# Performance work log

Measured on AMD Instinct MI355X. Metric: run time of the kernel, lower is better.

The kernel has to match this reference:

```python
import jax, jax.numpy as jnp
import numpy as np

B_IMG = 2
N_PROP = 2000
N_GT = 16
C_FEAT = 256
H_FEAT = 128
W_FEAT = 128
IMG = 1024.0
NUM_CLASSES = 2
BG_THRESH = 0.5          # fg==bg==0.5 -> BETWEEN_THRESHOLDS band is empty
BPI = 512                # batch_size_per_image
NUM_POS_MAX = int(BPI * 0.25)
ENC_W = (1.0, 1.0, 1.0, 1.0, 1.0)
SCALE = 1.0 / 8.0        # feature stride
POOL = 7
SR = 2                   # sampling_ratio
BETA = 1.0 / 9.0
HID = 1024


def _make_boxes(key, shape_prefix, img=IMG):
    kc, ks = jax.random.split(key)
    c = jax.random.uniform(kc, shape_prefix + (2,), minval=0.0, maxval=img)
    s = jax.random.uniform(ks, shape_prefix + (2,), minval=20.0, maxval=200.0)
    lo = jnp.clip(c - 0.5 * s, 0.0, img - 2.0)
    hi = jnp.clip(c + 0.5 * s, lo + 1.0, img)
    return jnp.concatenate([lo, hi], axis=-1)  # [.., x1,y1,x2,y2]


def setup_inputs():
    key = jax.random.key(0)
    ks = jax.random.split(key, 12)
    features = jax.random.normal(ks[0], (B_IMG, C_FEAT, H_FEAT, W_FEAT), dtype=jnp.float32)
    proposals = _make_boxes(ks[1], (B_IMG, N_PROP))
    gt_boxes = _make_boxes(ks[2], (B_IMG, N_GT))
    gt_labels = jax.random.randint(ks[3], (B_IMG, N_GT), 1, NUM_CLASSES, dtype=jnp.int32)
    ka, kb, kt = jax.random.split(ks[4], 3)
    a = jax.random.uniform(ka, (B_IMG, N_GT), minval=10.0, maxval=60.0)
    b = jax.random.uniform(kb, (B_IMG, N_GT), minval=5.0, maxval=30.0)
    th = jax.random.uniform(kt, (B_IMG, N_GT), minval=-np.pi / 2, maxval=np.pi / 2)
    exy = 0.5 * (gt_boxes[..., :2] + gt_boxes[..., 2:])
    gt_ellipses = jnp.stack([a, b, exy[..., 0], exy[..., 1], th], axis=-1)
    d_in = C_FEAT * POOL * POOL
    w1 = jax.random.normal(ks[5], (d_in, HID), dtype=jnp.float32) * 0.02
    b1 = jnp.zeros((HID,), jnp.float32)
    w2 = jax.random.normal(ks[6], (HID, HID), dtype=jnp.float32) * 0.02
    b2 = jnp.zeros((HID,), jnp.float32)
    wc = jax.random.normal(ks[7], (HID, NUM_CLASSES), dtype=jnp.float32) * 0.02
    bc = jnp.zeros((NUM_CLASSES,), jnp.float32)
    wr = jax.random.normal(ks[8], (HID, NUM_CLASSES * 6), dtype=jnp.float32) * 0.02
    br = jnp.zeros((NUM_CLASSES * 6,), jnp.float32)
    return dict(features=features, proposals=proposals, gt_boxes=gt_boxes,
                gt_labels=gt_labels, gt_ellipses=gt_ellipses,
                w1=w1, b1=b1, w2=w2, b2=b2, wc=wc, bc=bc, wr=wr, br=br)


def box_iou(b1, b2):  # [G,4], [P,4] -> [G,P]
    a1 = (b1[:, 2] - b1[:, 0]) * (b1[:, 3] - b1[:, 1])
    a2 = (b2[:, 2] - b2[:, 0]) * (b2[:, 3] - b2[:, 1])
    lt = jnp.maximum(b1[:, None, :2], b2[None, :, :2])
    rb = jnp.minimum(b1[:, None, 2:], b2[None, :, 2:])
    wh = jnp.clip(rb - lt, 0.0)
    inter = wh[..., 0] * wh[..., 1]
    return inter / (a1[:, None] + a2[None, :] - inter)


def encode_ellipses(ell, boxes):  # ell [..,5]=(a,b,cx,cy,theta), boxes [..,4] -> [..,6]
    a, b, ex, ey, th = (ell[..., i] for i in range(5))
    w = jnp.maximum(boxes[..., 2] - boxes[..., 0], 1.0)
    h = jnp.maximum(boxes[..., 3] - boxes[..., 1], 1.0)
    cx = 0.5 * (boxes[..., 0] + boxes[..., 2])
    cy = 0.5 * (boxes[..., 1] + boxes[..., 3])
    wx, wy, wa, wb, wt = ENC_W
    dx = wx * (ex - cx) / w
    dy = wy * (ey - cy) / h
    da = wa * jnp.log(jnp.maximum(2.0 * a, 1e-3) / w)
    db = wb * jnp.log(jnp.maximum(2.0 * b, 1e-3) / h)
    return jnp.stack([dx, dy, da, db, wt * jnp.sin(2.0 * th), wt * jnp.cos(2.0 * th)], axis=-1)


def roi_align(fmap, rois):  # [C,H,W], [R,4] -> [R,C,POOL,POOL]
    C, H, W = fmap.shape
    r = rois * SCALE
    x1, y1, x2, y2 = r[:, 0], r[:, 1], r[:, 2], r[:, 3]
    bw = jnp.maximum(x2 - x1, 1.0) / POOL
    bh = jnp.maximum(y2 - y1, 1.0) / POOL
    S = POOL * SR
    off = (jnp.arange(S, dtype=jnp.float32) + 0.5) / SR  # bin-unit sample offsets
    ys = jnp.clip(y1[:, None] + off[None, :] * bh[:, None], 0.0, H - 1.0)  # [R,S]
    xs = jnp.clip(x1[:, None] + off[None, :] * bw[:, None], 0.0, W - 1.0)
    y0 = jnp.clip(jnp.floor(ys), 0, H - 2).astype(jnp.int32)
    x0 = jnp.clip(jnp.floor(xs), 0, W - 2).astype(jnp.int32)
    ly = ys - y0
    lx = xs - x0
    Ya, Yb = y0[:, :, None], (y0 + 1)[:, :, None]  # [R,S,1]
    Xa, Xb = x0[:, None, :], (x0 + 1)[:, None, :]  # [R,1,S]
    v00 = fmap[:, Ya, Xa]; v01 = fmap[:, Ya, Xb]   # [C,R,S,S]
    v10 = fmap[:, Yb, Xa]; v11 = fmap[:, Yb, Xb]
    wy1 = ly[:, :, None]; wy0 = 1.0 - wy1
    wx1 = lx[:, None, :]; wx0 = 1.0 - wx1
    val = v00 * (wy0 * wx0) + v01 * (wy0 * wx1) + v10 * (wy1 * wx0) + v11 * (wy1 * wx1)
    R = rois.shape[0]
    pooled = val.reshape(C, R, POOL, SR, POOL, SR).mean(axis=(3, 5))
    return pooled.transpose(1, 0, 2, 3)


def reference(features, proposals, gt_boxes, gt_labels, gt_ellipses,
              w1, b1, w2, b2, wc, bc, wr, br):
    B = features.shape[0]
    # add_gt_proposals
    props = jnp.concatenate([proposals, gt_boxes], axis=1)            # [B,P,4]
    # assign_targets_to_proposals: IoU + Matcher (fg=bg=0.5)
    iou = jax.vmap(box_iou)(gt_boxes, props)                          # [B,G,P]
    matched_vals = iou.max(axis=1)
    matches = iou.argmax(axis=1)                                      # [B,P]
    lab = jnp.take_along_axis(gt_labels, matches, axis=1)
    lab = jnp.where(matched_vals < BG_THRESH, 0, lab)                 # background
    # BalancedPositiveNegativeSampler (deterministic, fixed-shape):
    # cap positives at NUM_POS_MAX by random rank, fill rest with random negatives
    rand = jax.random.uniform(jax.random.key(42), lab.shape)
    is_pos = lab > 0
    is_neg = lab == 0
    pos_s = jnp.where(is_pos, rand, -1e9)
    rank = jnp.argsort(jnp.argsort(-pos_s, axis=1), axis=1)
    capped = is_pos & (rank < NUM_POS_MAX)
    prio = jnp.where(capped, rand + 2.0, jnp.where(is_neg, rand, -1e9))
    _, idx = jax.lax.top_k(prio, BPI)                                 # [B,512]
    boxes = jnp.take_along_axis(props, idx[..., None], axis=1)        # [B,512,4]
    labels = jnp.take_along_axis(lab, idx, axis=1)                    # [B,512]
    m = jnp.take_along_axis(matches, idx, axis=1)
    ell = jnp.take_along_axis(gt_ellipses, m[..., None], axis=1)      # [B,512,5]
    targets = encode_ellipses(ell, boxes)                             # [B,512,6]
    # RoIAlign + TwoMLPHead + predictor
    pooled = jax.vmap(roi_align)(features, boxes)                     # [B,512,C,7,7]
    N = B * BPI
    x = pooled.reshape(N, -1)
    x = jax.nn.relu(x @ w1 + b1)
    x = jax.nn.relu(x @ w2 + b2)
    logits = x @ wc + bc                                              # [N,2]
    reg = (x @ wr + br).reshape(N, NUM_CLASSES, 6)
    # ellipse_rcnn_loss
    labels_f = labels.reshape(N)
    t = targets.reshape(N, 6)
    ce = -jnp.take_along_axis(jax.nn.log_softmax(logits, axis=-1), labels_f[:, None], axis=1).mean()
    pred = jnp.take_along_axis(reg, labels_f[:, None, None], axis=1)[:, 0]  # [N,6]
    d = jnp.abs(pred - t)
    sl1 = jnp.where(d < BETA, 0.5 * d * d / BETA, d - 0.5 * BETA)
    reg_loss = jnp.sum(sl1 * (labels_f > 0)[:, None].astype(sl1.dtype)) / N
    return jnp.stack([ce, reg_loss])
```

## Files before the change

### kernel.cpp

```cpp
#include <hip/hip_runtime.h>
#include <hip/hip_bf16.h>
#include <math.h>

#define B_IMG   2
#define N_PROP  2000
#define N_GT    16
#define NPROPS  2016
#define C_FEAT  256
#define H_FEAT  128
#define W_FEAT  128
#define HWF     (H_FEAT*W_FEAT)
#define POOL    7
#define BPI     512
#define NPOSMAX 128
#define NSEL    (B_IMG*BPI)
#define K1      (C_FEAT*POOL*POOL)
#define K1P     12800
#define HID     1024
#define NHEAD   14
#define SPLITK1 16
#define SPLITK2 4

typedef short bf16x8f __attribute__((ext_vector_type(8)));
typedef float f32x4f  __attribute__((ext_vector_type(4)));
typedef short short4v __attribute__((ext_vector_type(4)));

__device__ __forceinline__ void threefry2x32(unsigned k0, unsigned k1,
                                             unsigned& x0, unsigned& x1) {
  unsigned ks[3] = {k0, k1, k0 ^ k1 ^ 0x1BD11BDAu};
  const int R0[4] = {13, 15, 26, 6};
  const int R1[4] = {17, 29, 16, 24};
  x0 += ks[0]; x1 += ks[1];
#pragma unroll
  for (int g = 0; g < 5; g++) {
    const int* rot = (g & 1) ? R1 : R0;
#pragma unroll
    for (int r = 0; r < 4; r++) {
      x0 += x1;
      x1 = (x1 << rot[r]) | (x1 >> (32 - rot[r]));
      x1 ^= x0;
    }
    x0 += ks[(g + 1) % 3];
    x1 += ks[(g + 2) % 3] + (unsigned)(g + 1);
  }
}

__global__ __launch_bounds__(256) void k_sample(const float* __restrict__ proposals,
                                                const float* __restrict__ gt_boxes,
                                                const int* __restrict__ gt_labels,
                                                float* __restrict__ prio,
                                                int* __restrict__ plab,
                                                int* __restrict__ matches) {
  __shared__ float rs[NPROPS];
  __shared__ short pos_i[NPROPS];
  __shared__ float pos_r[NPROPS];
  __shared__ float gtb[N_GT * 4];
  __shared__ int   gtl[N_GT];
  __shared__ int   cnt;
  int b = blockIdx.x;
  int tid = threadIdx.x;
  int base = b * NPROPS;
  if (tid == 0) cnt = 0;
  if (tid < N_GT * 4) gtb[tid] = gt_boxes[b * N_GT * 4 + tid];
  if (tid < N_GT) gtl[tid] = gt_labels[b * N_GT + tid];
  __syncthreads();
  for (int i = tid; i < NPROPS; i += 256) {
    unsigned x0 = 0u, x1 = (unsigned)(base + i);
    threefry2x32(0u, 42u, x0, x1);
    unsigned bits = x0 ^ x1;
    float r = __uint_as_float((bits >> 9) | 0x3F800000u) - 1.0f;
    rs[i] = r;
    float p0, p1, p2, p3;
    if (i < N_PROP) {
      const float4 v = *(const float4*)(proposals + ((size_t)b * N_PROP + i) * 4);
      p0 = v.x; p1 = v.y; p2 = v.z; p3 = v.w;
    } else {
      const float* g = &gtb[(i - N_PROP) * 4];
      p0 = g[0]; p1 = g[1]; p2 = g[2]; p3 = g[3];
    }
    float a2 = (p2 - p0) * (p3 - p1);
    float best = -1.0f; int bg = 0;
#pragma unroll
    for (int g = 0; g < N_GT; g++) {
      float g0 = gtb[g * 4], g1 = gtb[g * 4 + 1], g2 = gtb[g * 4 + 2], g3 = gtb[g * 4 + 3];
      float a1 = (g2 - g0) * (g3 - g1);
      float wx = fmaxf(fminf(g2, p2) - fmaxf(g0, p0), 0.0f);
      float wy = fmaxf(fminf(g3, p3) - fmaxf(g1, p1), 0.0f);
      float inter = wx * wy;
      float iou = inter / (a1 + a2 - inter);
      if (iou > best) { best = iou; bg = g; }
    }
    matches[base + i] = bg;
    int lab = (best < 0.5f) ? 0 : gtl[bg];
    plab[base + i] = lab;
    if (lab > 0) {
      int s = atomicAdd(&cnt, 1);
      pos_i[s] = (short)i; pos_r[s] = r;
    }
  }
  __syncthreads();
  int P = cnt;
  for (int s = tid; s < P; s += 256) {
    int i = pos_i[s]; float ri = pos_r[s];
    int ch = 0;
    for (int j = 0; j < P; j++) {
      float rj = pos_r[j]; int ij = pos_i[j];
      ch += (rj > ri || (rj == ri && ij < i)) ? 1 : 0;
    }
    rs[i] = (ch < NPOSMAX) ? (ri + 2.0f) : -1000000000.0f;
  }
  __syncthreads();
  for (int i = tid; i < NPROPS; i += 256) prio[base + i] = rs[i];
}

__global__ __launch_bounds__(256) void k_select(const float* __restrict__ prio,
    const float* __restrict__ proposals, const float* __restrict__ gt_boxes,
    const int* __restrict__ matches, const int* __restrict__ plab,
    const float* __restrict__ gt_ell,
    float* __restrict__ sel_boxes, int* __restrict__ sel_labels,
    float* __restrict__ targets) {
  int tid = threadIdx.x;
  int wave = tid >> 6, lane = tid & 63;
  int b = blockIdx.y;
  int base = b * NPROPS;
  int i = blockIdx.x * 4 + wave;
  float pi = prio[base + i];
  int rank = 0;
  for (int j = lane; j < NPROPS; j += 64) {
    float pj = prio[base + j];
    rank += (pj > pi || (pj == pi && j < i)) ? 1 : 0;
  }
#pragma unroll
  for (int off = 32; off > 0; off >>= 1) rank += __shfl_down(rank, off);
  if (lane != 0 || rank >= BPI) return;
  int slot = b * BPI + rank;
  float p0, p1, p2, p3;
  if (i < N_PROP) {
    const float* p = proposals + ((size_t)b * N_PROP + i) * 4;
    p0 = p[0]; p1 = p[1]; p2 = p[2]; p3 = p[3];
  } else {
    const float* p = gt_boxes + ((size_t)b * N_GT + (i - N_PROP)) * 4;
    p0 = p[0]; p1 = p[1]; p2 = p[2]; p3 = p[3];
  }
  sel_boxes[slot * 4 + 0] = p0;
  sel_boxes[slot * 4 + 1] = p1;
  sel_boxes[slot * 4 + 2] = p2;
  sel_boxes[slot * 4 + 3] = p3;
  int lb = plab[base + i];
  sel_labels[slot] = lb;
  int m = matches[base + i];
  const float* e = gt_ell + ((size_t)b * N_GT + m) * 5;
  float ea = e[0], eb = e[1], ex = e[2], ey = e[3], eth = e[4];
  float w = fmaxf(p2 - p0, 1.0f), h = fmaxf(p3 - p1, 1.0f);
  float cx = 0.5f * (p0 + p2), cy = 0.5f * (p1 + p3);
  float* t = targets + (size_t)slot * 6;
  t[0] = (ex - cx) / w;
  t[1] = (ey - cy) / h;
  t[2] = logf(fmaxf(2.0f * ea, 0.001f) / w);
  t[3] = logf(fmaxf(2.0f * eb, 0.001f) / h);
  t[4] = sinf(2.0f * eth);
  t[5] = cosf(2.0f * eth);
}

__global__ __launch_bounds__(256) void k_transpose(const float* __restrict__ in,
                                                   __hip_bfloat16* __restrict__ out) {
  __shared__ float tile[64][65];
  int b = blockIdx.z;
  int s0 = blockIdx.x * 64;
  int c0 = blockIdx.y * 64;
  const float* src = in + (size_t)b * C_FEAT * HWF;
  __hip_bfloat16* dst = out + (size_t)b * HWF * C_FEAT;
  int t = threadIdx.x;
  int hw4 = (t & 15) * 4;
  int cr  = t >> 4;
#pragma unroll
  for (int p = 0; p < 4; p++) {
    int c = cr + p * 16;
    float4 v = *(const float4*)(src + (size_t)(c0 + c) * HWF + s0 + hw4);
    tile[hw4 + 0][c] = v.x;
    tile[hw4 + 1][c] = v.y;
    tile[hw4 + 2][c] = v.z;
    tile[hw4 + 3][c] = v.w;
  }
  __syncthreads();
  int c4 = (t & 15) * 4;
  int hr = t >> 4;
#pragma unroll
  for (int p = 0; p < 4; p++) {
    int hw = hr + p * 16;
    __hip_bfloat16 o[4] = {__float2bfloat16(tile[hw][c4]), __float2bfloat16(tile[hw][c4 + 1]),
                           __float2bfloat16(tile[hw][c4 + 2]), __float2bfloat16(tile[hw][c4 + 3])};
    *(short4v*)(dst + (size_t)(s0 + hw) * C_FEAT + c0 + c4) = *(short4v*)o;
  }
}

template <int PERM>
__global__ __launch_bounds__(256) void k_castT(const float* __restrict__ W,
                                               __hip_bfloat16* __restrict__ WT,
                                               int Kout) {
  __shared__ float t[64][65];
  int p  = blockIdx.z;
  int c0 = blockIdx.x * 64;
  int n0 = blockIdx.y * 64;
  int tx = threadIdx.x & 63, ty = threadIdx.x >> 6;
#pragma unroll
  for (int i = ty; i < 64; i += 4) {
    int krow = PERM ? ((c0 + i) * 49 + p) : (c0 + i);
    t[i][tx] = W[(size_t)krow * HID + n0 + tx];
  }
  __syncthreads();
#pragma unroll
  for (int i = ty; i < 64; i += 4) {
    int kx = PERM ? (p * 256 + c0 + tx) : (c0 + tx);
    WT[(size_t)(n0 + i) * Kout + kx] = __float2bfloat16(t[tx][i]);
  }
}

__global__ __launch_bounds__(256) void k_pad(__hip_bfloat16* __restrict__ Xb,
                                             __hip_bfloat16* __restrict__ W1T) {
  __hip_bfloat16* buf = blockIdx.y ? W1T : Xb;
  int t = blockIdx.x * 256 + threadIdx.x;
  int row = t >> 6;
  int col4 = (t & 63) << 2;
  short4v z = {0, 0, 0, 0};
  *(short4v*)(buf + (size_t)row * K1P + K1 + col4) = z;
}

__global__ __launch_bounds__(256) void k_roialign(const __hip_bfloat16* __restrict__ featT,
                                                  const float* __restrict__ sel_boxes,
                                                  __hip_bfloat16* __restrict__ X) {
  int n = blockIdx.x;
  int py = blockIdx.y;
  int t = threadIdx.x;
  int lane = t & 63, sub = t >> 6;
  int c = lane << 2;
  int b = n >> 9;
  const float* bx = sel_boxes + (size_t)n * 4;
  float x1 = bx[0] * 0.125f, y1 = bx[1] * 0.125f;
  float x2 = bx[2] * 0.125f, y2 = bx[3] * 0.125f;
  float bw = fmaxf(x2 - x1, 1.0f) / 7.0f;
  float bh = fmaxf(y2 - y1, 1.0f) / 7.0f;
  const __hip_bfloat16* base = featT + (size_t)b * HWF * C_FEAT;
  int y0A[2]; float lyA[2];
#pragma unroll
  for (int sy = 0; sy < 2; sy++) {
    float off = ((float)(py * 2 + sy) + 0.5f) * 0.5f;
    float ys = fminf(fmaxf(y1 + off * bh, 0.0f), 127.0f);
    int y0 = (int)fminf(fmaxf(floorf(ys), 0.0f), 126.0f);
    y0A[sy] = y0; lyA[sy] = ys - (float)y0;
  }
#pragma unroll
  for (int pass = 0; pass < 2; pass++) {
    int px = sub + (pass << 2);
    if (px >= 7) break;
    float acc[4] = {0.0f, 0.0f, 0.0f, 0.0f};
#pragma unroll
    for (int sx = 0; sx < 2; sx++) {
      float off = ((float)(px * 2 + sx) + 0.5f) * 0.5f;
      float xs = fminf(fmaxf(x1 + off * bw, 0.0f), 127.0f);
      int x0 = (int)fminf(fmaxf(floorf(xs), 0.0f), 126.0f);
      float lx = xs - (float)x0;
#pragma unroll
      for (int sy = 0; sy < 2; sy++) {
        int y0 = y0A[sy]; float ly = lyA[sy];
        const __hip_bfloat16* p = base + ((size_t)(y0 * W_FEAT + x0)) * C_FEAT + c;
        short4v s00 = *(const short4v*)p;
        short4v s01 = *(const short4v*)(p + C_FEAT);
        short4v s10 = *(const short4v*)(p + W_FEAT * C_FEAT);
        short4v s11 = *(const short4v*)(p + W_FEAT * C_FEAT + C_FEAT);
        float w00 = (1.0f - ly) * (1.0f - lx), w01 = (1.0f - ly) * lx;
        float w10 = ly * (1.0f - lx), w11 = ly * lx;
#pragma unroll
        for (int q = 0; q < 4; q++) {
          float v00 = __uint_as_float(((unsigned)(unsigned short)s00[q]) << 16);
          float v01 = __uint_as_float(((unsigned)(unsigned short)s01[q]) << 16);
          float v10 = __uint_as_float(((unsigned)(unsigned short)s10[q]) << 16);
          float v11 = __uint_as_float(((unsigned)(unsigned short)s11[q]) << 16);
          acc[q] += v00 * w00 + v01 * w01 + v10 * w10 + v11 * w11;
        }
      }
    }
    __hip_bfloat16 o[4] = {__float2bfloat16(acc[0] * 0.25f), __float2bfloat16(acc[1] * 0.25f),
                           __float2bfloat16(acc[2] * 0.25f), __float2bfloat16(acc[3] * 0.25f)};
    *(short4v*)&X[(size_t)n * K1P + (size_t)(py * 7 + px) * C_FEAT + c] = *(short4v*)o;
  }
}

__device__ __forceinline__ void gld_lds16(const __hip_bfloat16* g, __hip_bfloat16* l) {
  __builtin_amdgcn_global_load_lds(
      (const __attribute__((address_space(1))) void*)g,
      (__attribute__((address_space(3))) void*)l, 16, 0, 0);
}

template <int MODE>
__global__ __launch_bounds__(MODE == 1 ? 512 : 256)
void k_mfma_gemm(const __hip_bfloat16* __restrict__ A,
                 const __hip_bfloat16* __restrict__ BT,
                 float* __restrict__ P, int K, int KC) {
  const int AM  = (MODE == 1) ? 256 : 128;
  const int TPB = AM * 2;
  __shared__ __align__(16) __hip_bfloat16 As[AM * 32];
  __shared__ __align__(16) __hip_bfloat16 Bs[128 * 32];
  int lin = blockIdx.x;
  int n0, m0, kz;
  if (MODE == 1) {
    int c = lin & 7, h = lin >> 8, q = (lin >> 3) & 31;
    kz = c + (h << 3);
    n0 = (q & 7) * 128;
    m0 = (q >> 3) * 256;
  } else {
    int c = lin & 7;
    kz = c >> 1;
    int q = (lin >> 3) + ((c & 1) << 5);
    n0 = (q & 7) * 128;
    m0 = (q >> 3) * 128;
  }
  int tid = threadIdx.x;
  int kbeg = kz * KC;
  int srow = tid >> 2;
  int scs  = tid & 3;
  int sg   = scs ^ (srow & 3);
  int scol = sg << 3;
  int wave = tid >> 6, lane = tid & 63;
  const int WMW = AM / 64;
  int wm = (wave % WMW) * 64, wn = (wave / WMW) * 64;
  int lm = lane & 15, quad = lane >> 4;
  int fco = ((quad ^ (lm & 3)) << 3);
  f32x4f acc[4][4] = {};
  for (int k0 = kbeg; k0 < kbeg + KC; k0 += 32) {
    __syncthreads();
#pragma unroll
    for (int r0 = 0; r0 < AM; r0 += TPB / 4)
      gld_lds16(A + (size_t)(m0 + r0 + srow) * K + k0 + scol, &As[(r0 + srow) * 32 + scs * 8]);
#pragma unroll
    for (int r0 = 0; r0 < 128; r0 += TPB / 4)
      gld_lds16(BT + (size_t)(n0 + r0 + srow) * K + k0 + scol, &Bs[(r0 + srow) * 32 + scs * 8]);
    __syncthreads();
    bf16x8f af[4], bf[4];
#pragma unroll
    for (int i = 0; i < 4; i++)
      af[i] = *(const bf16x8f*)&As[(wm + i * 16 + lm) * 32 + fco];
#pragma unroll
    for (int j = 0; j < 4; j++)
      bf[j] = *(const bf16x8f*)&Bs[(wn + j * 16 + lm) * 32 + fco];
#pragma unroll
    for (int i = 0; i < 4; i++)
#pragma unroll
      for (int j = 0; j < 4; j++)
        acc[i][j] = __builtin_amdgcn_mfma_f32_16x16x32_bf16(af[i], bf[j], acc[i][j], 0, 0, 0);
  }
#pragma unroll
  for (int i = 0; i < 4; i++)
#pragma unroll
    for (int j = 0; j < 4; j++) {
      float* base = P + ((size_t)kz << 20)
                      + (size_t)(m0 + wm + i * 16 + quad * 4) * HID
                      + (n0 + wn + j * 16 + lm);
#pragma unroll
      for (int r = 0; r < 4; r++) base[(size_t)r * HID] = acc[i][j][r];
    }
}

template <int Z>
__global__ __launch_bounds__(256) void k_reduce(const float* __restrict__ P,
                                                const float* __restrict__ bias,
                                                __hip_bfloat16* __restrict__ O) {
  int idx4 = blockIdx.x * 256 + threadIdx.x;
  int m = idx4 >> 8;
  int n4 = (idx4 & 255) << 2;
  float4 s = *(const float4*)(bias + n4);
#pragma unroll
  for (int z = 0; z < Z; z++) {
    float4 p = *(const float4*)(P + ((size_t)z << 20) + ((size_t)m << 10) + n4);
    s.x += p.x; s.y += p.y; s.z += p.z; s.w += p.w;
  }
  __hip_bfloat16 t[4] = {__float2bfloat16(fmaxf(s.x, 0.0f)), __float2bfloat16(fmaxf(s.y, 0.0f)),
                         __float2bfloat16(fmaxf(s.z, 0.0f)), __float2bfloat16(fmaxf(s.w, 0.0f))};
  *(short4v*)(O + ((size_t)m << 10) + n4) = *(short4v*)t;
}

__global__ __launch_bounds__(256) void k_reduce_head(const float* __restrict__ P,
                                                     const float* __restrict__ bias,
                                                     const float* __restrict__ wc,
                                                     const float* __restrict__ bc,
                                                     const float* __restrict__ wr,
                                                     const float* __restrict__ br,
                                                     float* __restrict__ Y) {
  __shared__ float part[4][NHEAD];
  int m = blockIdx.x, tid = threadIdx.x;
  int n4 = tid << 2;
  float4 s = *(const float4*)(bias + n4);
#pragma unroll
  for (int z = 0; z < SPLITK2; z++) {
    float4 p = *(const float4*)(P + ((size_t)z << 20) + ((size_t)m << 10) + n4);
    s.x += p.x; s.y += p.y; s.z += p.z; s.w += p.w;
  }
  float hv4[4] = {fmaxf(s.x, 0.0f), fmaxf(s.y, 0.0f), fmaxf(s.z, 0.0f), fmaxf(s.w, 0.0f)};
  float a[NHEAD];
#pragma unroll
  for (int j = 0; j < NHEAD; j++) a[j] = 0.0f;
#pragma unroll
  for (int q = 0; q < 4; q++) {
    int kk = n4 + q;
    float hv = hv4[q];
    float2 wcv = *(const float2*)(wc + kk * 2);
    float4 w0 = *(const float4*)(wr + kk * 12);
    float4 w1 = *(const float4*)(wr + kk * 12 + 4);
    float4 w2 = *(const float4*)(wr + kk * 12 + 8);
    a[0] += hv * wcv.x;  a[1] += hv * wcv.y;
    a[2] += hv * w0.x;   a[3] += hv * w0.y;  a[4] += hv * w0.z;  a[5] += hv * w0.w;
    a[6] += hv * w1.x;   a[7] += hv * w1.y;  a[8] += hv * w1.z;  a[9] += hv * w1.w;
    a[10] += hv * w2.x;  a[11] += hv * w2.y; a[12] += hv * w2.z; a[13] += hv * w2.w;
  }
#pragma unroll
  for (int j = 0; j < NHEAD; j++)
#pragma unroll
    for (int off = 32; off > 0; off >>= 1) a[j] += __shfl_down(a[j], off);
  int wave = tid >> 6, lane = tid & 63;
  if (lane == 0)
#pragma unroll
    for (int j = 0; j < NHEAD; j++) part[wave][j] = a[j];
  __syncthreads();
  if (tid < NHEAD) {
    float v = part[0][tid] + part[1][tid] + part[2][tid] + part[3][tid];
    Y[(size_t)m * NHEAD + tid] = v + ((tid < 2) ? bc[tid] : br[tid - 2]);
  }
}

__global__ __launch_bounds__(1024) void k_loss(const float* __restrict__ Y,
                                               const int* __restrict__ sel_labels,
                                               const float* __restrict__ T,
                                               float* __restrict__ out) {
  __shared__ float sc[1024];
  __shared__ float sr[1024];
  int n = threadIdx.x;
  float l0 = Y[(size_t)n * NHEAD + 0], l1 = Y[(size_t)n * NHEAD + 1];
  int lb = sel_labels[n];
  float mx = fmaxf(l0, l1);
  float lse = mx + logf(expf(l0 - mx) + expf(l1 - mx));
  float ce = lse - (lb ? l1 : l0);
  float reg = 0.0f;
  if (lb > 0) {
    const float beta = 1.0f / 9.0f;
    const float* pr = Y + (size_t)n * NHEAD + 2 + lb * 6;
    const float* t = T + (size_t)n * 6;
#pragma unroll
    for (int j = 0; j < 6; j++) {
      float d = fabsf(pr[j] - t[j]);
      reg += (d < beta) ? (0.5f * d * d / beta) : (d - 0.5f * beta);
    }
  }
  sc[n] = ce; sr[n] = reg;
  __syncthreads();
  for (int s = 512; s > 0; s >>= 1) {
    if (n < s) { sc[n] += sc[n + s]; sr[n] += sr[n + s]; }
    __syncthreads();
  }
  if (n == 0) {
    out[0] = sc[0] * (1.0f / 1024.0f);
    out[1] = sr[0] * (1.0f / 1024.0f);
  }
}

extern "C" void kernel_launch(void* const* d_in, const int* in_sizes, int n_in,
                              void* d_out, int out_size, void* d_ws, size_t ws_size,
                              hipStream_t stream) {
  const float* features  = (const float*)d_in[0];
  const float* proposals = (const float*)d_in[1];
  const float* gt_boxes  = (const float*)d_in[2];
  const int*   gt_labels = (const int*)d_in[3];
  const float* gt_ell    = (const float*)d_in[4];
  const float* w1 = (const float*)d_in[5];
  const float* b1 = (const float*)d_in[6];
  const float* w2 = (const float*)d_in[7];
  const float* b2 = (const float*)d_in[8];
  const float* wc = (const float*)d_in[9];
  const float* bc = (const float*)d_in[10];
  const float* wr = (const float*)d_in[11];
  const float* br = (const float*)d_in[12];
  float* out = (float*)d_out;

  char* ws = (char*)d_ws;
  size_t off = 0;
  auto take = [&](size_t bytes) -> void* {
    void* p = ws + off;
    off = (off + bytes + 255) & ~(size_t)255;
    return p;
  };
  float* P = (float*)take((size_t)SPLITK1 * HID * HID * 4);
  __hip_bfloat16* featT = (__hip_bfloat16*)P;
  __hip_bfloat16* Xb  = (__hip_bfloat16*)take((size_t)NSEL * K1P * 2);
  float* Y   = (float*)Xb;
  __hip_bfloat16* W1T = (__hip_bfloat16*)take((size_t)HID * K1P * 2);
  __hip_bfloat16* W2T = (__hip_bfloat16*)take((size_t)HID * HID * 2);
  __hip_bfloat16* H1b = (__hip_bfloat16*)take((size_t)NSEL * HID * 2);
  int*   matches   = (int*)take((size_t)B_IMG * NPROPS * 4);
  int*   plab      = (int*)take((size_t)B_IMG * NPROPS * 4);
  float* prio      = (float*)take((size_t)B_IMG * NPROPS * 4);
  float* sel_boxes = (float*)take((size_t)NSEL * 4 * 4);
  int*   sel_lab   = (int*)take((size_t)NSEL * 4);
  float* targets   = (float*)take((size_t)NSEL * 6 * 4);

  k_sample<<<B_IMG, 256, 0, stream>>>(proposals, gt_boxes, gt_labels, prio, plab, matches);
  k_pad<<<dim3(256, 2), 256, 0, stream>>>(Xb, W1T);
  k_transpose<<<dim3(HWF / 64, C_FEAT / 64, B_IMG), 256, 0, stream>>>(features, featT);
  k_castT<1><<<dim3(C_FEAT / 64, HID / 64, 49), 256, 0, stream>>>(w1, W1T, K1P);
  k_castT<0><<<dim3(HID / 64, HID / 64, 1), 256, 0, stream>>>(w2, W2T, HID);
  k_select<<<dim3(NPROPS / 4, B_IMG), 256, 0, stream>>>(prio, proposals, gt_boxes,
                                                        matches, plab, gt_ell,
                                                        sel_boxes, sel_lab, targets);
  k_roialign<<<dim3(NSEL, POOL), 256, 0, stream>>>(featT, sel_boxes, Xb);

  k_mfma_gemm<1><<<512, 512, 0, stream>>>(Xb, W1T, P, K1P, K1P / SPLITK1);
  k_reduce<SPLITK1><<<1024, 256, 0, stream>>>(P, b1, H1b);
  k_mfma_gemm<2><<<256, 256, 0, stream>>>(H1b, W2T, P, HID, HID / SPLITK2);
  k_reduce_head<<<1024, 256, 0, stream>>>(P, b2, wc, bc, wr, br, Y);

  k_loss<<<1, 1024, 0, stream>>>(Y, sel_lab, targets, out);
}
```

Measured before the change: 287.3 us.

## Fuse preprocessing kernels and store split-K partials as tiled bf16

Merges the sampling, feature transpose, weight cast and padding kernels into one launch that dispatches on block index, cutting launch overhead and serial gaps. GEMM split-K partials are now written as bf16 in a fragment-native tiled layout instead of fp32 row-major, which halves partial-sum traffic and makes the stores contiguous. The reducers are rewritten to index that layout. The second GEMM uses split-K 8 instead of 4 for more blocks. Rounding partials to bf16 before reduction loses accuracy.

Result: faster. 239.2 us (-16.7%).

```diff
diff --git a/kernel.cpp b/kernel.cpp
--- a/kernel.cpp
+++ b/kernel.cpp
@@ -19,7 +19,7 @@
 #define HID     1024
 #define NHEAD   14
 #define SPLITK1 16
-#define SPLITK2 4
+#define SPLITK2 8
 
 typedef short bf16x8f __attribute__((ext_vector_type(8)));
 typedef float f32x4f  __attribute__((ext_vector_type(4)));
@@ -45,72 +45,151 @@
   }
 }
 
-__global__ __launch_bounds__(256) void k_sample(const float* __restrict__ proposals,
-                                                const float* __restrict__ gt_boxes,
-                                                const int* __restrict__ gt_labels,
-                                                float* __restrict__ prio,
-                                                int* __restrict__ plab,
-                                                int* __restrict__ matches) {
-  __shared__ float rs[NPROPS];
-  __shared__ short pos_i[NPROPS];
-  __shared__ float pos_r[NPROPS];
-  __shared__ float gtb[N_GT * 4];
-  __shared__ int   gtl[N_GT];
-  __shared__ int   cnt;
-  int b = blockIdx.x;
+#define PRE_SAMPLE   2
+#define PRE_TRANS    (PRE_SAMPLE + 2048)
+#define PRE_CAST1    (PRE_TRANS + 3136)
+#define PRE_CAST0    (PRE_CAST1 + 256)
+#define PRE_TOTAL    (PRE_CAST0 + 512)
+
+__global__ __launch_bounds__(256) void k_pre(const float* __restrict__ proposals,
+                                             const float* __restrict__ gt_boxes,
+                                             const int* __restrict__ gt_labels,
+                                             const float* __restrict__ features,
+                                             const float* __restrict__ w1,
+                                             const float* __restrict__ w2,
+                                             float* __restrict__ prio,
+                                             int* __restrict__ plab,
+                                             int* __restrict__ matches,
+                                             __hip_bfloat16* __restrict__ featT,
+                                             __hip_bfloat16* __restrict__ W1T,
+                                             __hip_bfloat16* __restrict__ W2T,
+                                             __hip_bfloat16* __restrict__ Xb) {
+  __shared__ __align__(16) char smem[20800];
+  int bid = blockIdx.x;
   int tid = threadIdx.x;
-  int base = b * NPROPS;
-  if (tid == 0) cnt = 0;
-  if (tid < N_GT * 4) gtb[tid] = gt_boxes[b * N_GT * 4 + tid];
-  if (tid < N_GT) gtl[tid] = gt_labels[b * N_GT + tid];
-  __syncthreads();
-  for (int i = tid; i < NPROPS; i += 256) {
-    unsigned x0 = 0u, x1 = (unsigned)(base + i);
-    threefry2x32(0u, 42u, x0, x1);
-    unsigned bits = x0 ^ x1;
-    float r = __uint_as_float((bits >> 9) | 0x3F800000u) - 1.0f;
-    rs[i] = r;
-    float p0, p1, p2, p3;
-    if (i < N_PROP) {
-      const float4 v = *(const float4*)(proposals + ((size_t)b * N_PROP + i) * 4);
-      p0 = v.x; p1 = v.y; p2 = v.z; p3 = v.w;
-    } else {
-      const float* g = &gtb[(i - N_PROP) * 4];
-      p0 = g[0]; p1 = g[1]; p2 = g[2]; p3 = g[3];
-    }
-    float a2 = (p2 - p0) * (p3 - p1);
-    float best = -1.0f; int bg = 0;
-#pragma unroll
-    for (int g = 0; g < N_GT; g++) {
-      float g0 = gtb[g * 4], g1 = gtb[g * 4 + 1], g2 = gtb[g * 4 + 2], g3 = gtb[g * 4 + 3];
-      float a1 = (g2 - g0) * (g3 - g1);
-      float wx = fmaxf(fminf(g2, p2) - fmaxf(g0, p0), 0.0f);
-      float wy = fmaxf(fminf(g3, p3) - fmaxf(g1, p1), 0.0f);
-      float inter = wx * wy;
-      float iou = inter / (a1 + a2 - inter);
-      if (iou > best) { best = iou; bg = g; }
-    }
-    matches[base + i] = bg;
-    int lab = (best < 0.5f) ? 0 : gtl[bg];
-    plab[base + i] = lab;
-    if (lab > 0) {
-      int s = atomicAdd(&cnt, 1);
-      pos_i[s] = (short)i; pos_r[s] = r;
-    }
-  }
-  __syncthreads();
-  int P = cnt;
-  for (int s = tid; s < P; s += 256) {
-    int i = pos_i[s]; float ri = pos_r[s];
-    int ch = 0;
-    for (int j = 0; j < P; j++) {
-      float rj = pos_r[j]; int ij = pos_i[j];
-      ch += (rj > ri || (rj == ri && ij < i)) ? 1 : 0;
-    }
-    rs[i] = (ch < NPOSMAX) ? (ri + 2.0f) : -1000000000.0f;
-  }
-  __syncthreads();
-  for (int i = tid; i < NPROPS; i += 256) prio[base + i] = rs[i];
+  if (bid < PRE_SAMPLE) {
+    float* rs    = (float*)smem;
+    float* pos_r = (float*)(smem + 8064);
+    short* pos_i = (short*)(smem + 16128);
+    float* gtb   = (float*)(smem + 20160);
+    int*   gtl   = (int*)(smem + 20416);
+    int*   cnt   = (int*)(smem + 20480);
+    int b = bid;
+    int base = b * NPROPS;
+    if (tid == 0) *cnt = 0;
+    if (tid < N_GT * 4) gtb[tid] = gt_boxes[b * N_GT * 4 + tid];
+    if (tid < N_GT) gtl[tid] = gt_labels[b * N_GT + tid];
+    __syncthreads();
+    for (int i = tid; i < NPROPS; i += 256) {
+      unsigned x0 = 0u, x1 = (unsigned)(base + i);
+      threefry2x32(0u, 42u, x0, x1);
+      unsigned bits = x0 ^ x1;
+      float r = __uint_as_float((bits >> 9) | 0x3F800000u) - 1.0f;
+      rs[i] = r;
+      float p0, p1, p2, p3;
+      if (i < N_PROP) {
+        const float4 v = *(const float4*)(proposals + ((size_t)b * N_PROP + i) * 4);
+        p0 = v.x; p1 = v.y; p2 = v.z; p3 = v.w;
+      } else {
+        const float* g = &gtb[(i - N_PROP) * 4];
+        p0 = g[0]; p1 = g[1]; p2 = g[2]; p3 = g[3];
+      }
+      float a2 = (p2 - p0) * (p3 - p1);
+      float best = -1.0f; int bg = 0;
+#pragma unroll
+      for (int g = 0; g < N_GT; g++) {
+        float g0 = gtb[g*4], g1 = gtb[g*4+1], g2 = gtb[g*4+2], g3 = gtb[g*4+3];
+        float a1 = (g2 - g0) * (g3 - g1);
+        float wx = fmaxf(fminf(g2, p2) - fmaxf(g0, p0), 0.0f);
+        float wy = fmaxf(fminf(g3, p3) - fmaxf(g1, p1), 0.0f);
+        float inter = wx * wy;
+        float iou = inter / (a1 + a2 - inter);
+        if (iou > best) { best = iou; bg = g; }
+      }
+      matches[base + i] = bg;
+      int lab = (best < 0.5f) ? 0 : gtl[bg];
+      plab[base + i] = lab;
+      if (lab > 0) {
+        int s = atomicAdd(cnt, 1);
+        pos_i[s] = (short)i; pos_r[s] = r;
+      }
+    }
+    __syncthreads();
+    int P = *cnt;
+    for (int s = tid; s < P; s += 256) {
+      int i = pos_i[s]; float ri = pos_r[s];
+      int ch = 0;
+      for (int j = 0; j < P; j++) {
+        float rj = pos_r[j]; int ij = pos_i[j];
+        ch += (rj > ri || (rj == ri && ij < i)) ? 1 : 0;
+      }
+      rs[i] = (ch < NPOSMAX) ? (ri + 2.0f) : -1000000000.0f;
+    }
+    __syncthreads();
+    for (int i = tid; i < NPROPS; i += 256) prio[base + i] = rs[i];
+  } else if (bid < PRE_TRANS) {
+    float (*tile)[65] = (float(*)[65])smem;
+    int t = bid - PRE_SAMPLE;
+    int b = t >> 10;
+    int rem = t & 1023;
+    int c0 = (rem >> 8) * 64;
+    int s0 = (rem & 255) * 64;
+    const float* src = features + (size_t)b * C_FEAT * HWF;
+    __hip_bfloat16* dst = featT + (size_t)b * HWF * C_FEAT;
+    int hw4 = (tid & 15) * 4, cr = tid >> 4;
+#pragma unroll
+    for (int p = 0; p < 4; p++) {
+      int c = cr + p * 16;
+      float4 v = *(const float4*)(src + (size_t)(c0 + c) * HWF + s0 + hw4);
+      tile[hw4 + 0][c] = v.x; tile[hw4 + 1][c] = v.y;
+      tile[hw4 + 2][c] = v.z; tile[hw4 + 3][c] = v.w;
+    }
+    __syncthreads();
+    int c4 = (tid & 15) * 4, hr = tid >> 4;
+#pragma unroll
+    for (int p = 0; p < 4; p++) {
+      int hw = hr + p * 16;
+      __hip_bfloat16 o[4] = {__float2bfloat16(tile[hw][c4]), __float2bfloat16(tile[hw][c4+1]),
+                             __float2bfloat16(tile[hw][c4+2]), __float2bfloat16(tile[hw][c4+3])};
+      *(short4v*)(dst + (size_t)(s0 + hw) * C_FEAT + c0 + c4) = *(short4v*)o;
+    }
+  } else if (bid < PRE_CAST1) {
+    float (*tile)[65] = (float(*)[65])smem;
+    int t = bid - PRE_TRANS;
+    int p = t >> 6;
+    int rem = t & 63;
+    int c0 = (rem & 3) * 64;
+    int n0 = (rem >> 2) * 64;
+    int tx = tid & 63, ty = tid >> 6;
+#pragma unroll
+    for (int i = ty; i < 64; i += 4)
+      tile[i][tx] = w1[(size_t)((c0 + i) * 49 + p) * HID + n0 + tx];
+    __syncthreads();
+#pragma unroll
+    for (int i = ty; i < 64; i += 4)
+      W1T[(size_t)(n0 + i) * K1P + p * 256 + c0 + tx] = __float2bfloat16(tile[tx][i]);
+  } else if (bid < PRE_CAST0) {
+    float (*tile)[65] = (float(*)[65])smem;
+    int t = bid - PRE_CAST1;
+    int c0 = (t & 15) * 64;
+    int n0 = (t >> 4) * 64;
+    int tx = tid & 63, ty = tid >> 6;
+#pragma unroll
+    for (int i = ty; i < 64; i += 4)
+      tile[i][tx] = w2[(size_t)(c0 + i) * HID + n0 + tx];
+    __syncthreads();
+#pragma unroll
+    for (int i = ty; i < 64; i += 4)
+      W2T[(size_t)(n0 + i) * HID + c0 + tx] = __float2bfloat16(tile[tx][i]);
+  } else {
+    int t = bid - PRE_CAST0;
+    __hip_bfloat16* buf = (t >> 8) ? W1T : Xb;
+    int tt = (t & 255) * 256 + tid;
+    int row = tt >> 6;
+    int col4 = (tt & 63) << 2;
+    short4v z = {0, 0, 0, 0};
+    *(short4v*)(buf + (size_t)row * K1P + K1 + col4) = z;
+  }
 }
 
 __global__ __launch_bounds__(256) void k_select(const float* __restrict__ prio,
@@ -162,70 +241,6 @@
   t[5] = cosf(2.0f * eth);
 }
 
-__global__ __launch_bounds__(256) void k_transpose(const float* __restrict__ in,
-                                                   __hip_bfloat16* __restrict__ out) {
-  __shared__ float tile[64][65];
-  int b = blockIdx.z;
-  int s0 = blockIdx.x * 64;
-  int c0 = blockIdx.y * 64;
-  const float* src = in + (size_t)b * C_FEAT * HWF;
-  __hip_bfloat16* dst = out + (size_t)b * HWF * C_FEAT;
-  int t = threadIdx.x;
-  int hw4 = (t & 15) * 4;
-  int cr  = t >> 4;
-#pragma unroll
-  for (int p = 0; p < 4; p++) {
-    int c = cr + p * 16;
-    float4 v = *(const float4*)(src + (size_t)(c0 + c) * HWF + s0 + hw4);
-    tile[hw4 + 0][c] = v.x;
-    tile[hw4 + 1][c] = v.y;
-    tile[hw4 + 2][c] = v.z;
-    tile[hw4 + 3][c] = v.w;
-  }
-  __syncthreads();
-  int c4 = (t & 15) * 4;
-  int hr = t >> 4;
-#pragma unroll
-  for (int p = 0; p < 4; p++) {
-    int hw = hr + p * 16;
-    __hip_bfloat16 o[4] = {__float2bfloat16(tile[hw][c4]), __float2bfloat16(tile[hw][c4 + 1]),
-                           __float2bfloat16(tile[hw][c4 + 2]), __float2bfloat16(tile[hw][c4 + 3])};
-    *(short4v*)(dst + (size_t)(s0 + hw) * C_FEAT + c0 + c4) = *(short4v*)o;
-  }
-}
-
-template <int PERM>
-__global__ __launch_bounds__(256) void k_castT(const float* __restrict__ W,
-                                               __hip_bfloat16* __restrict__ WT,
-                                               int Kout) {
-  __shared__ float t[64][65];
-  int p  = blockIdx.z;
-  int c0 = blockIdx.x * 64;
-  int n0 = blockIdx.y * 64;
-  int tx = threadIdx.x & 63, ty = threadIdx.x >> 6;
-#pragma unroll
-  for (int i = ty; i < 64; i += 4) {
-    int krow = PERM ? ((c0 + i) * 49 + p) : (c0 + i);
-    t[i][tx] = W[(size_t)krow * HID + n0 + tx];
-  }
-  __syncthreads();
-#pragma unroll
-  for (int i = ty; i < 64; i += 4) {
-    int kx = PERM ? (p * 256 + c0 + tx) : (c0 + tx);
-    WT[(size_t)(n0 + i) * Kout + kx] = __float2bfloat16(t[tx][i]);
-  }
-}
-
-__global__ __launch_bounds__(256) void k_pad(__hip_bfloat16* __restrict__ Xb,
-                                             __hip_bfloat16* __restrict__ W1T) {
-  __hip_bfloat16* buf = blockIdx.y ? W1T : Xb;
-  int t = blockIdx.x * 256 + threadIdx.x;
-  int row = t >> 6;
-  int col4 = (t & 63) << 2;
-  short4v z = {0, 0, 0, 0};
-  *(short4v*)(buf + (size_t)row * K1P + K1 + col4) = z;
-}
-
 __global__ __launch_bounds__(256) void k_roialign(const __hip_bfloat16* __restrict__ featT,
                                                   const float* __restrict__ sel_boxes,
                                                   __hip_bfloat16* __restrict__ X) {
@@ -296,7 +311,7 @@
 __global__ __launch_bounds__(MODE == 1 ? 512 : 256)
 void k_mfma_gemm(const __hip_bfloat16* __restrict__ A,
                  const __hip_bfloat16* __restrict__ BT,
-                 float* __restrict__ P, int K, int KC) {
+                 __hip_bfloat16* __restrict__ Pb, int K, int KC) {
   const int AM  = (MODE == 1) ? 256 : 128;
   const int TPB = AM * 2;
   __shared__ __align__(16) __hip_bfloat16 As[AM * 32];
@@ -309,9 +324,8 @@
     n0 = (q & 7) * 128;
     m0 = (q >> 3) * 256;
   } else {
-    int c = lin & 7;
-    kz = c >> 1;
-    int q = (lin >> 3) + ((c & 1) << 5);
+    kz = lin & 7;
+    int q = lin >> 3;
     n0 = (q & 7) * 128;
     m0 = (q >> 3) * 128;
   }
@@ -349,37 +363,46 @@
       for (int j = 0; j < 4; j++)
         acc[i][j] = __builtin_amdgcn_mfma_f32_16x16x32_bf16(af[i], bf[j], acc[i][j], 0, 0, 0);
   }
+  int tileoff = (MODE == 1) ? (((m0 >> 8) * 8 + (n0 >> 7)) * 32768)
+                            : (((m0 >> 7) * 8 + (n0 >> 7)) * 16384);
+  __hip_bfloat16* dst = Pb + ((size_t)kz << 20) + tileoff + wave * 4096 + lane * 4;
 #pragma unroll
   for (int i = 0; i < 4; i++)
 #pragma unroll
     for (int j = 0; j < 4; j++) {
-      float* base = P + ((size_t)kz << 20)
-                      + (size_t)(m0 + wm + i * 16 + quad * 4) * HID
-                      + (n0 + wn + j * 16 + lm);
-#pragma unroll
-      for (int r = 0; r < 4; r++) base[(size_t)r * HID] = acc[i][j][r];
-    }
-}
-
-template <int Z>
-__global__ __launch_bounds__(256) void k_reduce(const float* __restrict__ P,
-                                                const float* __restrict__ bias,
-                                                __hip_bfloat16* __restrict__ O) {
-  int idx4 = blockIdx.x * 256 + threadIdx.x;
-  int m = idx4 >> 8;
-  int n4 = (idx4 & 255) << 2;
-  float4 s = *(const float4*)(bias + n4);
-#pragma unroll
-  for (int z = 0; z < Z; z++) {
-    float4 p = *(const float4*)(P + ((size_t)z << 20) + ((size_t)m << 10) + n4);
-    s.x += p.x; s.y += p.y; s.z += p.z; s.w += p.w;
-  }
-  __hip_bfloat16 t[4] = {__float2bfloat16(fmaxf(s.x, 0.0f)), __float2bfloat16(fmaxf(s.y, 0.0f)),
-                         __float2bfloat16(fmaxf(s.z, 0.0f)), __float2bfloat16(fmaxf(s.w, 0.0f))};
-  *(short4v*)(O + ((size_t)m << 10) + n4) = *(short4v*)t;
-}
-
-__global__ __launch_bounds__(256) void k_reduce_head(const float* __restrict__ P,
+      __hip_bfloat16 o[4] = {__float2bfloat16(acc[i][j][0]), __float2bfloat16(acc[i][j][1]),
+                             __float2bfloat16(acc[i][j][2]), __float2bfloat16(acc[i][j][3])};
+      *(short4v*)(dst + (i * 4 + j) * 256) = *(short4v*)o;
+    }
+}
+
+__global__ __launch_bounds__(256) void k_reduce16(const __hip_bfloat16* __restrict__ Pb,
+                                                  const float* __restrict__ bias,
+                                                  __hip_bfloat16* __restrict__ O) {
+  int m4 = blockIdx.x >> 2;
+  int n  = (blockIdx.x & 3) * 256 + threadIdx.x;
+  int m0i = m4 >> 6, wavem = (m4 >> 4) & 3, i = (m4 >> 2) & 3, quad = m4 & 3;
+  int n0i = n >> 7, wn = (n >> 6) & 1, j = (n >> 4) & 3, lm = n & 15;
+  int wave = wavem + wn * 4;
+  int elem = (m0i * 8 + n0i) * 32768 + wave * 4096 + (i * 4 + j) * 256 + (quad * 16 + lm) * 4;
+  float s0 = 0.0f, s1 = 0.0f, s2 = 0.0f, s3 = 0.0f;
+#pragma unroll
+  for (int z = 0; z < SPLITK1; z++) {
+    short4v v = *(const short4v*)(Pb + ((size_t)z << 20) + elem);
+    s0 += __uint_as_float(((unsigned)(unsigned short)v[0]) << 16);
+    s1 += __uint_as_float(((unsigned)(unsigned short)v[1]) << 16);
+    s2 += __uint_as_float(((unsigned)(unsigned short)v[2]) << 16);
+    s3 += __uint_as_float(((unsigned)(unsigned short)v[3]) << 16);
+  }
+  float bv = bias[n];
+  int m = m4 * 4;
+  O[(size_t)(m + 0) * HID + n] = __float2bfloat16(fmaxf(s0 + bv, 0.0f));
+  O[(size_t)(m + 1) * HID + n] = __float2bfloat16(fmaxf(s1 + bv, 0.0f));
+  O[(size_t)(m + 2) * HID + n] = __float2bfloat16(fmaxf(s2 + bv, 0.0f));
+  O[(size_t)(m + 3) * HID + n] = __float2bfloat16(fmaxf(s3 + bv, 0.0f));
+}
+
+__global__ __launch_bounds__(256) void k_reduce_head(const __hip_bfloat16* __restrict__ Pb,
                                                      const float* __restrict__ bias,
                                                      const float* __restrict__ wc,
                                                      const float* __restrict__ bc,
@@ -388,25 +411,26 @@
                                                      float* __restrict__ Y) {
   __shared__ float part[4][NHEAD];
   int m = blockIdx.x, tid = threadIdx.x;
-  int n4 = tid << 2;
-  float4 s = *(const float4*)(bias + n4);
-#pragma unroll
-  for (int z = 0; z < SPLITK2; z++) {
-    float4 p = *(const float4*)(P + ((size_t)z << 20) + ((size_t)m << 10) + n4);
-    s.x += p.x; s.y += p.y; s.z += p.z; s.w += p.w;
-  }
-  float hv4[4] = {fmaxf(s.x, 0.0f), fmaxf(s.y, 0.0f), fmaxf(s.z, 0.0f), fmaxf(s.w, 0.0f)};
+  int m0i = m >> 7, wavem = (m >> 6) & 1, fi = (m >> 4) & 3, quad = (m >> 2) & 3, r = m & 3;
   float a[NHEAD];
 #pragma unroll
   for (int j = 0; j < NHEAD; j++) a[j] = 0.0f;
 #pragma unroll
-  for (int q = 0; q < 4; q++) {
-    int kk = n4 + q;
-    float hv = hv4[q];
-    float2 wcv = *(const float2*)(wc + kk * 2);
-    float4 w0 = *(const float4*)(wr + kk * 12);
-    float4 w1 = *(const float4*)(wr + kk * 12 + 4);
-    float4 w2 = *(const float4*)(wr + kk * 12 + 8);
+  for (int nn = 0; nn < 4; nn++) {
+    int n = nn * 256 + tid;
+    int n0i = n >> 7, wn = (n >> 6) & 1, fj = (n >> 4) & 3, lm = n & 15;
+    int wave = wavem + wn * 2;
+    int elem = (m0i * 8 + n0i) * 16384 + wave * 4096 + (fi * 4 + fj) * 256
+             + (quad * 16 + lm) * 4 + r;
+    float s = 0.0f;
+#pragma unroll
+    for (int z = 0; z < SPLITK2; z++)
+      s += __uint_as_float(((unsigned)*(const unsigned short*)(Pb + ((size_t)z << 20) + elem)) << 16);
+    float hv = fmaxf(s + bias[n], 0.0f);
+    float2 wcv = *(const float2*)(wc + n * 2);
+    float4 w0 = *(const float4*)(wr + n * 12);
+    float4 w1 = *(const float4*)(wr + n * 12 + 4);
+    float4 w2 = *(const float4*)(wr + n * 12 + 8);
     a[0] += hv * wcv.x;  a[1] += hv * wcv.y;
     a[2] += hv * w0.x;   a[3] += hv * w0.y;  a[4] += hv * w0.z;  a[5] += hv * w0.w;
     a[6] += hv * w1.x;   a[7] += hv * w1.y;  a[8] += hv * w1.z;  a[9] += hv * w1.w;
@@ -487,10 +511,10 @@
     off = (off + bytes + 255) & ~(size_t)255;
     return p;
   };
-  float* P = (float*)take((size_t)SPLITK1 * HID * HID * 4);
-  __hip_bfloat16* featT = (__hip_bfloat16*)P;
+  __hip_bfloat16* Pb = (__hip_bfloat16*)take((size_t)SPLITK1 * (1 << 20) * 2);
+  __hip_bfloat16* featT = Pb;
   __hip_bfloat16* Xb  = (__hip_bfloat16*)take((size_t)NSEL * K1P * 2);
-  float* Y   = (float*)Xb;
+  float* Y = (float*)Xb;
   __hip_bfloat16* W1T = (__hip_bfloat16*)take((size_t)HID * K1P * 2);
   __hip_bfloat16* W2T = (__hip_bfloat16*)take((size_t)HID * HID * 2);
   __hip_bfloat16* H1b = (__hip_bfloat16*)take((size_t)NSEL * HID * 2);
@@ -501,20 +525,18 @@
   int*   sel_lab   = (int*)take((size_t)NSEL * 4);
   float* targets   = (float*)take((size_t)NSEL * 6 * 4);
 
-  k_sample<<<B_IMG, 256, 0, stream>>>(proposals, gt_boxes, gt_labels, prio, plab, matches);
-  k_pad<<<dim3(256, 2), 256, 0, stream>>>(Xb, W1T);
-  k_transpose<<<dim3(HWF / 64, C_FEAT / 64, B_IMG), 256, 0, stream>>>(features, featT);
-  k_castT<1><<<dim3(C_FEAT / 64, HID / 64, 49), 256, 0, stream>>>(w1, W1T, K1P);
-  k_castT<0><<<dim3(HID / 64, HID / 64, 1), 256, 0, stream>>>(w2, W2T, HID);
+  k_pre<<<PRE_TOTAL, 256, 0, stream>>>(proposals, gt_boxes, gt_labels, features,
+                                       w1, w2, prio, plab, matches,
+                                       featT, W1T, W2T, Xb);
   k_select<<<dim3(NPROPS / 4, B_IMG), 256, 0, stream>>>(prio, proposals, gt_boxes,
                                                         matches, plab, gt_ell,
                                                         sel_boxes, sel_lab, targets);
   k_roialign<<<dim3(NSEL, POOL), 256, 0, stream>>>(featT, sel_boxes, Xb);
 
-  k_mfma_gemm<1><<<512, 512, 0, stream>>>(Xb, W1T, P, K1P, K1P / SPLITK1);
-  k_reduce<SPLITK1><<<1024, 256, 0, stream>>>(P, b1, H1b);
-  k_mfma_gemm<2><<<256, 256, 0, stream>>>(H1b, W2T, P, HID, HID / SPLITK2);
-  k_reduce_head<<<1024, 256, 0, stream>>>(P, b2, wc, bc, wr, br, Y);
+  k_mfma_gemm<1><<<512, 512, 0, stream>>>(Xb, W1T, Pb, K1P, K1P / SPLITK1);
+  k_reduce16<<<1024, 256, 0, stream>>>(Pb, b1, H1b);
+  k_mfma_gemm<2><<<512, 256, 0, stream>>>(H1b, W2T, Pb, HID, HID / SPLITK2);
+  k_reduce_head<<<1024, 256, 0, stream>>>(Pb, b2, wc, bc, wr, br, Y);
 
   k_loss<<<1, 1024, 0, stream>>>(Y, sel_lab, targets, out);
 }
```
